# Optimization experiments

Hardware: AMD Instinct MI355X
Metric: run time of the kernel (lower is better)

The kernel has to match this reference:

```python
import jax, jax.numpy as jnp
import numpy as np
from jax import lax

B, C, H, W = 8, 128, 128, 128


def setup_inputs() -> dict:
    key = jax.random.key(0)
    ks = jax.random.split(key, 10)
    s = 0.02
    return {
        "x": jax.random.normal(ks[0], (B, C, H, W), jnp.float32),
        "ln_w": jnp.ones((C,), jnp.float32),
        "ln_b": jnp.zeros((C,), jnp.float32),
        "qkv_w": jax.random.normal(ks[1], (3 * C, C, 1, 1), jnp.float32) * s,
        "qkv_b": jnp.zeros((3 * C,), jnp.float32),
        "dw_w": jax.random.normal(ks[2], (3 * C, 1, 3, 3), jnp.float32) * s,
        "dw_b": jnp.zeros((3 * C,), jnp.float32),
        "proj_w": jax.random.normal(ks[3], (C, C, 1, 1), jnp.float32) * s,
        "proj_b": jnp.zeros((C,), jnp.float32),
        "temp1": jnp.ones((1, 1), jnp.float32),
        "temp2": jnp.ones((1, 1), jnp.float32),
    }


def reference(x, ln_w, ln_b, qkv_w, qkv_b, dw_w, dw_b, proj_w, proj_b, temp1, temp2):
    Cd = x.shape[1]

    def ln(t):  # WithBias LayerNorm over channel dim (unbiased=False var)
        mu = t.mean(axis=1, keepdims=True)
        var = ((t - mu) ** 2).mean(axis=1, keepdims=True)
        return (t - mu) / jnp.sqrt(var + 1e-5) * ln_w[None, :, None, None] + ln_b[None, :, None, None]

    def conv1(t, w, b):  # 1x1 conv
        return jnp.einsum('bchw,oc->bohw', t, w[:, :, 0, 0]) + b[None, :, None, None]

    def dwc(t):  # depthwise 3x3, pad 1
        y = lax.conv_general_dilated(t, dw_w, (1, 1), ((1, 1), (1, 1)),
                                     dimension_numbers=('NCHW', 'OIHW', 'NCHW'),
                                     feature_group_count=t.shape[1])
        return y + dw_b[None, :, None, None]

    def l2n(t):  # F.normalize over last axis, eps=1e-12
        return t / jnp.maximum(jnp.linalg.norm(t, axis=-1, keepdims=True), 1e-12)

    # ---- stage 1: pool over H, attention over W (channel-pooled) ----
    qkv = dwc(conv1(ln(x), qkv_w, qkv_b))
    q1, k1, v1 = qkv[:, :Cd], qkv[:, Cd:2 * Cd], qkv[:, 2 * Cd:]
    q1 = l2n(q1.mean(axis=2)[:, None])           # [B,1,C,W]
    k1 = l2n(k1.max(axis=2)[:, None])            # [B,1,C,W]
    attn1 = jax.nn.softmax(jnp.einsum('bocw,bocv->bowv', q1, k1) * temp1, axis=-1)  # [B,1,W,W]
    out1 = jnp.einsum('bchw,bowv->bchv', v1, attn1)
    out1 = x + conv1(out1, proj_w, proj_b)

    # ---- stage 2: pool over C, attention over H ----
    qkv = dwc(conv1(ln(out1), qkv_w, qkv_b))
    q2, k2, v2 = qkv[:, :Cd], qkv[:, Cd:2 * Cd], qkv[:, 2 * Cd:]
    q2 = l2n(q2.mean(axis=1)[:, None])           # [B,1,H,W]
    k2 = l2n(k2.mean(axis=1)[:, None])           # [B,1,H,W]
    attn2 = jax.nn.softmax(jnp.einsum('bohw,bogw->bohg', q2, k2) * temp2, axis=-1)  # [B,1,H,H]
    out2 = jnp.einsum('bchw,bohg->bcgw', v2, attn2)  # = (v^T @ attn)^T
    out = conv1(out2, proj_w, proj_b) + out1
    return out
```

## Files before the change

kernel.cpp:

```cpp
#include <hip/hip_runtime.h>

typedef __attribute__((ext_vector_type(8))) short bf16x8;
typedef __attribute__((ext_vector_type(4))) float f32x4;
typedef __attribute__((ext_vector_type(4))) unsigned short us4;
typedef __attribute__((ext_vector_type(4))) unsigned int u32x4;

static constexpr int CC = 128, NN = 16384;
static constexpr int O3 = 384;
static constexpr long long CN  = (long long)CC * NN;
static constexpr long long O3N = (long long)O3 * NN;

__device__ __forceinline__ float wave_sum(float v) {
  for (int o = 32; o; o >>= 1) v += __shfl_xor(v, o);
  return v;
}
__device__ __forceinline__ float wave_max(float v) {
  for (int o = 32; o; o >>= 1) v = fmaxf(v, __shfl_xor(v, o));
  return v;
}
__device__ __forceinline__ unsigned short f2bf(float f) {
  unsigned u = __float_as_uint(f);
  u += 0x7FFF + ((u >> 16) & 1);
  return (unsigned short)(u >> 16);
}
__device__ __forceinline__ float bf2f(unsigned short h) {
  return __uint_as_float((unsigned)h << 16);
}

__global__ __launch_bounds__(64) void k_prep(const float* __restrict__ qkvw,
                                             const float* __restrict__ qkvb,
                                             const float* __restrict__ lnw,
                                             const float* __restrict__ lnb,
                                             const float* __restrict__ projw,
                                             unsigned short* __restrict__ Aq,
                                             unsigned short* __restrict__ Ap,
                                             float* __restrict__ Svec,
                                             float* __restrict__ bias2) {
  int o = blockIdx.x, t = threadIdx.x;
  if (o < O3) {
    float w0 = qkvw[o * 128 + t], w1 = qkvw[o * 128 + t + 64];
    unsigned short h0 = f2bf(w0 * lnw[t]), h1 = f2bf(w1 * lnw[t + 64]);
    Aq[o * 128 + t] = h0; Aq[o * 128 + t + 64] = h1;
    float s = wave_sum(bf2f(h0) + bf2f(h1));
    float bs = wave_sum(w0 * lnb[t] + w1 * lnb[t + 64]);
    if (t == 0) { Svec[o] = s; bias2[o] = qkvb[o] + bs; }
  } else {
    int r = o - O3;
    Ap[r * 128 + t] = f2bf(projw[r * 128 + t]);
    Ap[r * 128 + t + 64] = f2bf(projw[r * 128 + t + 64]);
  }
}

__global__ __launch_bounds__(256, 2) void k_qkv_mfma(
    const float* __restrict__ x, const float* __restrict__ mu, const float* __restrict__ rs,
    const unsigned short* __restrict__ Aq, const float* __restrict__ Svec,
    const float* __restrict__ bias2, unsigned short* __restrict__ out, int b0, int useg) {
  __shared__ unsigned short Bs[64 * 128];
  __shared__ float muL[64], rsL[64];
  int bz = blockIdx.z, bg = b0 + bz;
  int n0 = blockIdx.x * 64;
  int t = threadIdx.x, w = t >> 6, l = t & 63;
  int lr = l & 15, lg = l >> 4;
  const float* xb = x + (size_t)bg * CN + n0;

  bf16x8 afr[6][4];
  {
    const unsigned short* Abase = Aq + (size_t)(96 * w + lr) * 128 + lg * 8;
#pragma unroll
    for (int i = 0; i < 6; ++i)
#pragma unroll
      for (int ks = 0; ks < 4; ++ks)
        afr[i][ks] = *(const bf16x8*)&Abase[(size_t)(16 * i) * 128 + ks * 32];
  }

  {
    int n = t & 63, cb = t >> 6;
    float xr[32];
#pragma unroll
    for (int g = 0; g < 4; ++g)
#pragma unroll
      for (int q = 0; q < 8; ++q)
        xr[g * 8 + q] = xb[(size_t)((cb * 4 + g) * 8 + q) * NN + n];
#pragma unroll
    for (int g = 0; g < 4; ++g) {
      int c8 = (cb * 4 + g) * 8;
      unsigned pk[4];
#pragma unroll
      for (int q = 0; q < 4; ++q) {
        unsigned short a = f2bf(xr[g * 8 + 2 * q]);
        unsigned short b = f2bf(xr[g * 8 + 2 * q + 1]);
        pk[q] = (unsigned)a | ((unsigned)b << 16);
      }
      int c8s = c8 ^ ((n & 7) << 3);
      *(u32x4*)&Bs[n * 128 + c8s] = *(const u32x4*)pk;
    }
  }
  __syncthreads();

  if (!useg) {
    int p = t >> 2, sub = t & 3;
    float s1 = 0.f, s2 = 0.f;
#pragma unroll
    for (int b2 = 0; b2 < 4; ++b2) {
      int c8 = (sub * 4 + b2) * 8;
      int c8s = c8 ^ ((p & 7) << 3);
      bf16x8 v = *(const bf16x8*)&Bs[p * 128 + c8s];
#pragma unroll
      for (int q = 0; q < 8; ++q) {
        float f = bf2f((unsigned short)v[q]);
        s1 += f; s2 += f * f;
      }
    }
    s1 += __shfl_xor(s1, 1); s2 += __shfl_xor(s2, 1);
    s1 += __shfl_xor(s1, 2); s2 += __shfl_xor(s2, 2);
    if (sub == 0) {
      float m = s1 * (1.f / 128.f);
      muL[p] = m;
      rsL[p] = rsqrtf(s2 * (1.f / 128.f) - m * m + 1e-5f);
    }
  }
  __syncthreads();

  f32x4 acc[6][4];
#pragma unroll
  for (int i = 0; i < 6; ++i)
#pragma unroll
    for (int j = 0; j < 4; ++j) acc[i][j] = (f32x4){0.f, 0.f, 0.f, 0.f};
#pragma unroll
  for (int ks = 0; ks < 4; ++ks) {
    bf16x8 bfr[4];
#pragma unroll
    for (int j = 0; j < 4; ++j) {
      int row = 16 * j + lr;
      int col = (ks * 32 + lg * 8) ^ ((lr & 7) << 3);
      bfr[j] = *(const bf16x8*)&Bs[row * 128 + col];
    }
#pragma unroll
    for (int i = 0; i < 6; ++i)
#pragma unroll
      for (int j = 0; j < 4; ++j)
        acc[i][j] = __builtin_amdgcn_mfma_f32_16x16x32_bf16(afr[i][ks], bfr[j], acc[i][j], 0, 0, 0);
  }

  float rsv[4], muv[4];
#pragma unroll
  for (int j = 0; j < 4; ++j) {
    int nl = 16 * j + lr;
    if (useg) {
      rsv[j] = rs[(size_t)bg * NN + n0 + nl];
      muv[j] = mu[(size_t)bg * NN + n0 + nl];
    } else {
      rsv[j] = rsL[nl];
      muv[j] = muL[nl];
    }
  }
#pragma unroll
  for (int i = 0; i < 6; ++i) {
    int ob = 96 * w + 16 * i + lg * 4;
    float sv[4], bv[4];
#pragma unroll
    for (int r2 = 0; r2 < 4; ++r2) { sv[r2] = Svec[ob + r2]; bv[r2] = bias2[ob + r2]; }
#pragma unroll
    for (int j = 0; j < 4; ++j) {
      int n = n0 + 16 * j + lr;
      unsigned short* op = out + (size_t)bz * O3N + n;
#pragma unroll
      for (int r2 = 0; r2 < 4; ++r2)
        op[(size_t)(ob + r2) * NN] = f2bf(rsv[j] * (acc[i][j][r2] - muv[j] * sv[r2]) + bv[r2]);
    }
  }
}

__global__ __launch_bounds__(1024) void k_dwc(unsigned short* __restrict__ buf,
                                              const float* __restrict__ dww,
                                              const float* __restrict__ dwb,
                                              float* __restrict__ qm,
                                              float* __restrict__ km,
                                              int b0, int stage) {
  __shared__ unsigned short pl[130 * 144];
  __shared__ float red[32 * 128];
  int o = blockIdx.x, bz = blockIdx.y, bg = b0 + bz;
  int t = threadIdx.x;
  unsigned short* base = buf + (size_t)bz * O3N + (size_t)o * NN;
  unsigned* pl32 = (unsigned*)pl;

  for (int i = t; i < 1168; i += 1024) {
    int idx;
    if (i < 72) idx = i;
    else if (i < 144) idx = 129 * 72 + (i - 72);
    else { int j = i - 144; int row = (j >> 3) + 1; int s = j & 7;
           idx = row * 72 + (s < 4 ? s : 64 + s); }
    pl32[idx] = 0u;
  }
  __syncthreads();
#pragma unroll
  for (int r = 0; r < 2; ++r) {
    int idx = r * 1024 + t;
    int row = idx >> 4, c8 = (idx & 15) * 8;
    *(u32x4*)&pl[(row + 1) * 144 + 8 + c8] = *(const u32x4*)&base[row * 128 + c8];
  }
  __syncthreads();

  const float* wg = dww + o * 9;
  float w00 = wg[0], w01 = wg[1], w02 = wg[2];
  float w10 = wg[3], w11 = wg[4], w12 = wg[5];
  float w20 = wg[6], w21 = wg[7], w22 = wg[8];
  float bias = dwb[o];
  int mode = (stage == 0) ? (o < 128 ? 1 : (o < 256 ? 2 : 0)) : 0;
  int hh0 = t >> 5, w0 = (t & 31) * 4;
  float csum[4] = {0.f, 0.f, 0.f, 0.f};
  float cmax[4] = {-1e30f, -1e30f, -1e30f, -1e30f};

#pragma unroll
  for (int g = 0; g < 4; ++g) {
    int h = g * 32 + hh0;
    float a0 = bias, a1 = bias, a2 = bias, a3 = bias;
#pragma unroll
    for (int dr = 0; dr < 3; ++dr) {
      const unsigned short* rp = &pl[(h + dr) * 144];
      us4 cA = *(const us4*)&rp[w0 + 4];
      us4 cB = *(const us4*)&rp[w0 + 8];
      us4 cC = *(const us4*)&rp[w0 + 12];
      float f0 = bf2f(cA[3]), f1 = bf2f(cB[0]), f2 = bf2f(cB[1]);
      float f3 = bf2f(cB[2]), f4 = bf2f(cB[3]), f5 = bf2f(cC[0]);
      float wr0 = (dr == 0) ? w00 : (dr == 1 ? w10 : w20);
      float wr1 = (dr == 0) ? w01 : (dr == 1 ? w11 : w21);
      float wr2 = (dr == 0) ? w02 : (dr == 1 ? w12 : w22);
      a0 += f0 * wr0 + f1 * wr1 + f2 * wr2;
      a1 += f1 * wr0 + f2 * wr1 + f3 * wr2;
      a2 += f2 * wr0 + f3 * wr1 + f4 * wr2;
      a3 += f3 * wr0 + f4 * wr1 + f5 * wr2;
    }
    if (mode == 0) {
      us4 ov;
      ov[0] = f2bf(a0); ov[1] = f2bf(a1); ov[2] = f2bf(a2); ov[3] = f2bf(a3);
      *(us4*)&base[g * 4096 + t * 4] = ov;
    } else if (mode == 1) {
      csum[0] += a0; csum[1] += a1; csum[2] += a2; csum[3] += a3;
    } else {
      cmax[0] = fmaxf(cmax[0], a0); cmax[1] = fmaxf(cmax[1], a1);
      cmax[2] = fmaxf(cmax[2], a2); cmax[3] = fmaxf(cmax[3], a3);
    }
  }

  if (mode) {
    int j = t >> 5;
#pragma unroll
    for (int dx = 0; dx < 4; ++dx)
      red[j * 128 + w0 + dx] = (mode == 1) ? csum[dx] : cmax[dx];
    __syncthreads();
    if (t < 128) {
      float v = red[t];
      if (mode == 1) {
        for (int jj = 1; jj < 32; ++jj) v += red[jj * 128 + t];
        qm[(size_t)bg * NN + o * 128 + t] = v * (1.f / 128.f);
      } else {
        for (int jj = 1; jj < 32; ++jj) v = fmaxf(v, red[jj * 128 + t]);
        km[(size_t)bg * NN + (o - 128) * 128 + t] = v;
      }
    }
  }
}

__global__ __launch_bounds__(256) void k_reduce2(const unsigned short* __restrict__ qkv,
                                                 float* __restrict__ qm, float* __restrict__ km,
                                                 int b0) {
  int bz = blockIdx.y;
  int n = blockIdx.x * 256 + threadIdx.x;
  const unsigned short* base = qkv + (size_t)bz * O3N + n;
  float sq = 0.f, sk = 0.f;
#pragma unroll 4
  for (int c = 0; c < 128; ++c) {
    sq += bf2f(base[(size_t)c * NN]);
    sk += bf2f(base[(size_t)(c + 128) * NN]);
  }
  size_t off = (size_t)(b0 + bz) * NN + n;
  qm[off] = sq * (1.f / 128.f);
  km[off] = sk * (1.f / 128.f);
}

__global__ void k_norm2(float* __restrict__ qm, float* __restrict__ km, int row0) {
  float* buf = blockIdx.y ? km : qm;
  int r = row0 + blockIdx.x, t = threadIdx.x;
  float* p = buf + (size_t)r * 128;
  float v0 = p[t], v1 = p[t + 64];
  float s = wave_sum(v0 * v0 + v1 * v1);
  float sc = 1.f / fmaxf(sqrtf(s), 1e-12f);
  p[t] = v0 * sc;
  p[t + 64] = v1 * sc;
}

__global__ void k_attn1(const float* __restrict__ qm, const float* __restrict__ km,
                        const float* __restrict__ temp, unsigned short* __restrict__ attnT,
                        int b0) {
  int bg = b0 + blockIdx.y;
  int i = blockIdx.x, t = threadIdx.x;
  const float* qb = qm + (size_t)bg * NN;
  const float* kb = km + (size_t)bg * NN;
  __shared__ float qcol[128];
  __shared__ float wred[2];
  qcol[t] = qb[t * 128 + i];
  __syncthreads();
  float s = 0.f;
#pragma unroll 4
  for (int k = 0; k < 128; ++k) s += qcol[k] * kb[k * 128 + t];
  s *= temp[0];
  int wid = t >> 6, lane = t & 63;
  float mx = wave_max(s);
  if (lane == 0) wred[wid] = mx;
  __syncthreads();
  mx = fmaxf(wred[0], wred[1]);
  float pv = __expf(s - mx);
  __syncthreads();
  float sm = wave_sum(pv);
  if (lane == 0) wred[wid] = sm;
  __syncthreads();
  float denom = wred[0] + wred[1];
  attnT[(size_t)bg * NN + (size_t)t * 128 + i] = f2bf(pv / denom);
}

__global__ void k_attn2(const float* __restrict__ qm, const float* __restrict__ km,
                        const float* __restrict__ temp, unsigned short* __restrict__ attnT,
                        int b0) {
  int bg = b0 + blockIdx.y;
  int i = blockIdx.x, t = threadIdx.x;
  const float* qb = qm + (size_t)bg * NN + i * 128;
  const float* kb = km + (size_t)bg * NN + (size_t)t * 128;
  __shared__ float qrow[128];
  __shared__ float wred[2];
  qrow[t] = qb[t];
  __syncthreads();
  float s = 0.f;
#pragma unroll 4
  for (int w = 0; w < 128; ++w) s += qrow[w] * kb[w];
  s *= temp[0];
  int wid = t >> 6, lane = t & 63;
  float mx = wave_max(s);
  if (lane == 0) wred[wid] = mx;
  __syncthreads();
  mx = fmaxf(wred[0], wred[1]);
  float pv = __expf(s - mx);
  __syncthreads();
  float sm = wave_sum(pv);
  if (lane == 0) wred[wid] = sm;
  __syncthreads();
  float denom = wred[0] + wred[1];
  attnT[(size_t)bg * NN + (size_t)t * 128 + i] = f2bf(pv / denom);
}

__global__ __launch_bounds__(256) void k_apply1_mfma(unsigned short* __restrict__ buf,
                                                     const unsigned short* __restrict__ attnT,
                                                     int b0) {
  __shared__ unsigned short Al[128 * 136];
  __shared__ unsigned short Bl[128 * 136];
  int bz = blockIdx.z, bg = b0 + bz;
  int m0 = blockIdx.x * 128;
  int t = threadIdx.x, w = t >> 6, l = t & 63, lr = l & 15, lg = l >> 4;
  const unsigned short* asrc = buf + (size_t)bz * O3N + (size_t)256 * NN + (size_t)m0 * 128;
  const unsigned short* bsrc = attnT + (size_t)bg * NN;
#pragma unroll
  for (int r = 0; r < 8; ++r) {
    int idx = r * 256 + t;
    int row = idx >> 4, c8 = (idx & 15) * 8;
    *(u32x4*)&Al[row * 136 + c8] = *(const u32x4*)&asrc[row * 128 + c8];
    *(u32x4*)&Bl[row * 136 + c8] = *(const u32x4*)&bsrc[row * 128 + c8];
  }
  __syncthreads();
  f32x4 acc[2][8];
#pragma unroll
  for (int i = 0; i < 2; ++i)
#pragma unroll
    for (int j = 0; j < 8; ++j) acc[i][j] = (f32x4){0.f, 0.f, 0.f, 0.f};
#pragma unroll
  for (int ks = 0; ks < 4; ++ks) {
    bf16x8 bfr[8];
#pragma unroll
    for (int j = 0; j < 8; ++j)
      bfr[j] = *(const bf16x8*)&Bl[(16 * j + lr) * 136 + ks * 32 + lg * 8];
#pragma unroll
    for (int i = 0; i < 2; ++i) {
      bf16x8 afr = *(const bf16x8*)&Al[(32 * w + 16 * i + lr) * 136 + ks * 32 + lg * 8];
#pragma unroll
      for (int j = 0; j < 8; ++j)
        acc[i][j] = __builtin_amdgcn_mfma_f32_16x16x32_bf16(afr, bfr[j], acc[i][j], 0, 0, 0);
    }
  }
  unsigned short* ob = buf + (size_t)bz * O3N;
#pragma unroll
  for (int i = 0; i < 2; ++i)
#pragma unroll
    for (int j = 0; j < 8; ++j)
#pragma unroll
      for (int r2 = 0; r2 < 4; ++r2) {
        int m = m0 + 32 * w + 16 * i + lg * 4 + r2;
        int n = 16 * j + lr;
        ob[(size_t)m * 128 + n] = f2bf(acc[i][j][r2]);
      }
}

__global__ __launch_bounds__(256) void k_apply2_mfma(unsigned short* __restrict__ buf,
                                                     const unsigned short* __restrict__ attnT,
                                                     int b0) {
  __shared__ unsigned short At[128 * 136];
  __shared__ unsigned short Bt[128 * 136];
  int bz = blockIdx.z, bg = b0 + bz, c = blockIdx.x;
  int t = threadIdx.x, w = t >> 6, l = t & 63, lr = l & 15, lg = l >> 4;
  const unsigned short* vsrc = buf + (size_t)bz * O3N + (size_t)(256 + c) * NN;
  const unsigned short* asrc = attnT + (size_t)bg * NN;
#pragma unroll
  for (int r = 0; r < 8; ++r) {
    int idx = r * 256 + t;
    int row = idx >> 4, c8 = (idx & 15) * 8;
    *(u32x4*)&At[row * 136 + c8] = *(const u32x4*)&asrc[row * 128 + c8];
    us4 lo = *(const us4*)&vsrc[row * 128 + c8];
    us4 hi = *(const us4*)&vsrc[row * 128 + c8 + 4];
#pragma unroll
    for (int q = 0; q < 4; ++q) {
      Bt[(c8 + q) * 136 + row] = lo[q];
      Bt[(c8 + 4 + q) * 136 + row] = hi[q];
    }
  }
  __syncthreads();
  f32x4 acc[2][8];
#pragma unroll
  for (int i = 0; i < 2; ++i)
#pragma unroll
    for (int j = 0; j < 8; ++j) acc[i][j] = (f32x4){0.f, 0.f, 0.f, 0.f};
#pragma unroll
  for (int ks = 0; ks < 4; ++ks) {
    bf16x8 bfr[8];
#pragma unroll
    for (int j = 0; j < 8; ++j)
      bfr[j] = *(const bf16x8*)&Bt[(16 * j + lr) * 136 + ks * 32 + lg * 8];
#pragma unroll
    for (int i = 0; i < 2; ++i) {
      bf16x8 afr = *(const bf16x8*)&At[(32 * w + 16 * i + lr) * 136 + ks * 32 + lg * 8];
#pragma unroll
      for (int j = 0; j < 8; ++j)
        acc[i][j] = __builtin_amdgcn_mfma_f32_16x16x32_bf16(afr, bfr[j], acc[i][j], 0, 0, 0);
    }
  }
  unsigned short* ob = buf + (size_t)bz * O3N + (size_t)c * NN;
#pragma unroll
  for (int i = 0; i < 2; ++i)
#pragma unroll
    for (int j = 0; j < 8; ++j)
#pragma unroll
      for (int r2 = 0; r2 < 4; ++r2) {
        int g = 32 * w + 16 * i + lg * 4 + r2;
        int n = 16 * j + lr;
        ob[(size_t)g * 128 + n] = f2bf(acc[i][j][r2]);
      }
}

__global__ __launch_bounds__(256) void k_proj_mfma(
    const unsigned short* __restrict__ tin, const unsigned short* __restrict__ Ap,
    const float* __restrict__ pb, const float* __restrict__ res,
    float* __restrict__ dst, float* __restrict__ mu, float* __restrict__ rs,
    int b0, int do_stats) {
  __shared__ unsigned short Bs2[64 * 128];
  __shared__ float red1[64 * 17];
  __shared__ float red2[64 * 17];
  int bz = blockIdx.z, bg = b0 + bz;
  int n0 = blockIdx.x * 64;
  int t = threadIdx.x, w = t >> 6, l = t & 63, lr = l & 15, lg = l >> 4;
  const unsigned short* tb = tin + (size_t)bz * O3N + n0;

  bf16x8 afr[2][4];
  {
    const unsigned short* Abase = Ap + (size_t)(32 * w + lr) * 128 + lg * 8;
#pragma unroll
    for (int i = 0; i < 2; ++i)
#pragma unroll
      for (int ks = 0; ks < 4; ++ks)
        afr[i][ks] = *(const bf16x8*)&Abase[(size_t)(16 * i) * 128 + ks * 32];
  }

  {
    int n = t & 63, cb = t >> 6;
    unsigned short vr[32];
#pragma unroll
    for (int g = 0; g < 4; ++g)
#pragma unroll
      for (int q = 0; q < 8; ++q)
        vr[g * 8 + q] = tb[(size_t)((cb * 4 + g) * 8 + q) * NN + n];
#pragma unroll
    for (int g = 0; g < 4; ++g) {
      int c8 = (cb * 4 + g) * 8;
      unsigned pk[4];
#pragma unroll
      for (int q = 0; q < 4; ++q)
        pk[q] = (unsigned)vr[g * 8 + 2 * q] | ((unsigned)vr[g * 8 + 2 * q + 1] << 16);
      int c8s = c8 ^ ((n & 7) << 3);
      *(u32x4*)&Bs2[n * 128 + c8s] = *(const u32x4*)pk;
    }
  }
  __syncthreads();

  f32x4 acc[2][4];
#pragma unroll
  for (int i = 0; i < 2; ++i)
#pragma unroll
    for (int j = 0; j < 4; ++j) acc[i][j] = (f32x4){0.f, 0.f, 0.f, 0.f};

#pragma unroll
  for (int ks = 0; ks < 4; ++ks) {
    bf16x8 bfr[4];
#pragma unroll
    for (int j = 0; j < 4; ++j) {
      int row = 16 * j + lr;
      int col = (ks * 32 + lg * 8) ^ ((lr & 7) << 3);
      bfr[j] = *(const bf16x8*)&Bs2[row * 128 + col];
    }
#pragma unroll
    for (int i = 0; i < 2; ++i)
#pragma unroll
      for (int j = 0; j < 4; ++j)
        acc[i][j] = __builtin_amdgcn_mfma_f32_16x16x32_bf16(afr[i][ks], bfr[j], acc[i][j], 0, 0, 0);
  }

  float s1p[4] = {0.f, 0.f, 0.f, 0.f}, s2p[4] = {0.f, 0.f, 0.f, 0.f};
#pragma unroll
  for (int i = 0; i < 2; ++i) {
    int ob = 32 * w + 16 * i + lg * 4;
    float bv[4];
#pragma unroll
    for (int r2 = 0; r2 < 4; ++r2) bv[r2] = pb[ob + r2];
#pragma unroll
    for (int j = 0; j < 4; ++j) {
      int n = n0 + 16 * j + lr;
#pragma unroll
      for (int r2 = 0; r2 < 4; ++r2) {
        size_t off = (size_t)bg * CN + (size_t)(ob + r2) * NN + n;
        float val = acc[i][j][r2] + bv[r2] + res[off];
        dst[off] = val;
        s1p[j] += val;
        s2p[j] += val * val;
      }
    }
  }
  if (do_stats) {
#pragma unroll
    for (int j = 0; j < 4; ++j) {
      red1[(16 * j + lr) * 17 + (w * 4 + lg)] = s1p[j];
      red2[(16 * j + lr) * 17 + (w * 4 + lg)] = s2p[j];
    }
    __syncthreads();
    if (t < 64) {
      float s1 = 0.f, s2 = 0.f;
#pragma unroll
      for (int kk = 0; kk < 16; ++kk) { s1 += red1[t * 17 + kk]; s2 += red2[t * 17 + kk]; }
      float m = s1 * (1.f / 128.f);
      float var = s2 * (1.f / 128.f) - m * m;
      mu[(size_t)bg * NN + n0 + t] = m;
      rs[(size_t)bg * NN + n0 + t] = rsqrtf(var + 1e-5f);
    }
  }
}

extern "C" void kernel_launch(void* const* d_in, const int* in_sizes, int n_in,
                              void* d_out, int out_size, void* d_ws, size_t ws_size,
                              hipStream_t stream) {
  (void)in_sizes; (void)n_in; (void)out_size;
  const float* x     = (const float*)d_in[0];
  const float* lnw   = (const float*)d_in[1];
  const float* lnb   = (const float*)d_in[2];
  const float* qkvw  = (const float*)d_in[3];
  const float* qkvb  = (const float*)d_in[4];
  const float* dww   = (const float*)d_in[5];
  const float* dwb   = (const float*)d_in[6];
  const float* projw = (const float*)d_in[7];
  const float* projb = (const float*)d_in[8];
  const float* temp1 = (const float*)d_in[9];
  const float* temp2 = (const float*)d_in[10];
  float* out = (float*)d_out;
  float* ws = (float*)d_ws;

  auto needBytes = [&](int nb) {
    return ((size_t)nb * (O3N / 2) + 4ull * 131072 + 65536 + 768 + 24576 + 8192) * 4;
  };
  int NB = 8;
  while (NB > 1 && ws_size < needBytes(NB)) NB >>= 1;
  if (ws_size < needBytes(1)) return;

  unsigned short* convbuf = (unsigned short*)ws;
  float* mu = ws + (size_t)NB * (O3N / 2);
  float* rs = mu + 131072;
  float* qm = rs + 131072;
  float* km = qm + 131072;
  unsigned short* attnT = (unsigned short*)(km + 131072);
  float* Svec  = (float*)(attnT + 8ull * NN);
  float* bias2 = Svec + 384;
  unsigned short* Aq = (unsigned short*)(bias2 + 384);
  unsigned short* Ap = Aq + 49152;

  k_prep<<<512, 64, 0, stream>>>(qkvw, qkvb, lnw, lnb, projw, Aq, Ap, Svec, bias2);

  for (int stage = 0; stage < 2; ++stage) {
    const float* src = stage ? out : x;
    for (int b0 = 0; b0 < 8; b0 += NB) {
      k_qkv_mfma<<<dim3(256, 1, NB), 256, 0, stream>>>(src, mu, rs, Aq, Svec, bias2, convbuf,
                                                       b0, stage);
      k_dwc<<<dim3(384, NB), 1024, 0, stream>>>(convbuf, dww, dwb, qm, km, b0, stage);
      if (stage == 1)
        k_reduce2<<<dim3(64, NB), 256, 0, stream>>>(convbuf, qm, km, b0);
      k_norm2<<<dim3(NB * 128, 2), 64, 0, stream>>>(qm, km, b0 * 128);
      if (stage == 0)
        k_attn1<<<dim3(128, NB), 128, 0, stream>>>(qm, km, temp1, attnT, b0);
      else
        k_attn2<<<dim3(128, NB), 128, 0, stream>>>(qm, km, temp2, attnT, b0);
      if (stage == 0)
        k_apply1_mfma<<<dim3(128, 1, NB), 256, 0, stream>>>(convbuf, attnT, b0);
      else
        k_apply2_mfma<<<dim3(128, 1, NB), 256, 0, stream>>>(convbuf, attnT, b0);
      const float* resp = stage ? out : x;
      k_proj_mfma<<<dim3(256, 1, NB), 256, 0, stream>>>(convbuf, Ap, projb, resp, out,
                                                        mu, rs, b0, stage == 0 ? 1 : 0);
    }
  }
}
```

Measured before the change: 311.7 us.

## Stage weight tiles in LDS and split QKV GEMM across output halves

The QKV 1x1-conv kernel no longer holds all 384x128 weight fragments in registers. Each block now covers 192 output channels, staged into padded shared memory, and the grid doubles along that axis. The proj kernel likewise loads its weight matrix into padded LDS instead of registers. The aim is to cut register pressure and raise occupancy, at the cost of reading and LayerNorm-converting each x tile twice and adding LDS traffic for A fragments.

```diff
diff --git a/kernel.cpp b/kernel.cpp
--- a/kernel.cpp
+++ b/kernel.cpp
@@ -51,28 +51,29 @@
   }
 }
 
-__global__ __launch_bounds__(256, 2) void k_qkv_mfma(
+__global__ __launch_bounds__(256) void k_qkv_mfma(
     const float* __restrict__ x, const float* __restrict__ mu, const float* __restrict__ rs,
     const unsigned short* __restrict__ Aq, const float* __restrict__ Svec,
     const float* __restrict__ bias2, unsigned short* __restrict__ out, int b0, int useg) {
+  __shared__ unsigned short As[192 * 136];
   __shared__ unsigned short Bs[64 * 128];
   __shared__ float muL[64], rsL[64];
   int bz = blockIdx.z, bg = b0 + bz;
-  int n0 = blockIdx.x * 64;
+  int m0 = blockIdx.x * 192;
+  int n0 = blockIdx.y * 64;
   int t = threadIdx.x, w = t >> 6, l = t & 63;
   int lr = l & 15, lg = l >> 4;
   const float* xb = x + (size_t)bg * CN + n0;
 
-  bf16x8 afr[6][4];
   {
-    const unsigned short* Abase = Aq + (size_t)(96 * w + lr) * 128 + lg * 8;
-#pragma unroll
-    for (int i = 0; i < 6; ++i)
-#pragma unroll
-      for (int ks = 0; ks < 4; ++ks)
-        afr[i][ks] = *(const bf16x8*)&Abase[(size_t)(16 * i) * 128 + ks * 32];
-  }
-
+    const unsigned short* Asrc = Aq + (size_t)m0 * 128;
+#pragma unroll
+    for (int r = 0; r < 12; ++r) {
+      int v = r * 256 + t;
+      int m = v >> 4, c8 = (v & 15) * 8;
+      *(u32x4*)&As[m * 136 + c8] = *(const u32x4*)&Asrc[m * 128 + c8];
+    }
+  }
   {
     int n = t & 63, cb = t >> 6;
     float xr[32];
@@ -121,9 +122,9 @@
   }
   __syncthreads();
 
-  f32x4 acc[6][4];
-#pragma unroll
-  for (int i = 0; i < 6; ++i)
+  f32x4 acc[3][4];
+#pragma unroll
+  for (int i = 0; i < 3; ++i)
 #pragma unroll
     for (int j = 0; j < 4; ++j) acc[i][j] = (f32x4){0.f, 0.f, 0.f, 0.f};
 #pragma unroll
@@ -136,10 +137,12 @@
       bfr[j] = *(const bf16x8*)&Bs[row * 128 + col];
     }
 #pragma unroll
-    for (int i = 0; i < 6; ++i)
+    for (int i = 0; i < 3; ++i) {
+      bf16x8 afr = *(const bf16x8*)&As[(48 * w + 16 * i + lr) * 136 + ks * 32 + lg * 8];
 #pragma unroll
       for (int j = 0; j < 4; ++j)
-        acc[i][j] = __builtin_amdgcn_mfma_f32_16x16x32_bf16(afr[i][ks], bfr[j], acc[i][j], 0, 0, 0);
+        acc[i][j] = __builtin_amdgcn_mfma_f32_16x16x32_bf16(afr, bfr[j], acc[i][j], 0, 0, 0);
+    }
   }
 
   float rsv[4], muv[4];
@@ -155,8 +158,8 @@
     }
   }
 #pragma unroll
-  for (int i = 0; i < 6; ++i) {
-    int ob = 96 * w + 16 * i + lg * 4;
+  for (int i = 0; i < 3; ++i) {
+    int ob = m0 + 48 * w + 16 * i + lg * 4;
     float sv[4], bv[4];
 #pragma unroll
     for (int r2 = 0; r2 < 4; ++r2) { sv[r2] = Svec[ob + r2]; bv[r2] = bias2[ob + r2]; }
@@ -458,6 +461,7 @@
     const float* __restrict__ pb, const float* __restrict__ res,
     float* __restrict__ dst, float* __restrict__ mu, float* __restrict__ rs,
     int b0, int do_stats) {
+  __shared__ unsigned short Al[128 * 136];
   __shared__ unsigned short Bs2[64 * 128];
   __shared__ float red1[64 * 17];
   __shared__ float red2[64 * 17];
@@ -466,16 +470,12 @@
   int t = threadIdx.x, w = t >> 6, l = t & 63, lr = l & 15, lg = l >> 4;
   const unsigned short* tb = tin + (size_t)bz * O3N + n0;
 
-  bf16x8 afr[2][4];
-  {
-    const unsigned short* Abase = Ap + (size_t)(32 * w + lr) * 128 + lg * 8;
-#pragma unroll
-    for (int i = 0; i < 2; ++i)
-#pragma unroll
-      for (int ks = 0; ks < 4; ++ks)
-        afr[i][ks] = *(const bf16x8*)&Abase[(size_t)(16 * i) * 128 + ks * 32];
-  }
-
+#pragma unroll
+  for (int r = 0; r < 8; ++r) {
+    int v = r * 256 + t;
+    int m = v >> 4, c8 = (v & 15) * 8;
+    *(u32x4*)&Al[m * 136 + c8] = *(const u32x4*)&Ap[m * 128 + c8];
+  }
   {
     int n = t & 63, cb = t >> 6;
     unsigned short vr[32];
@@ -513,10 +513,12 @@
       bfr[j] = *(const bf16x8*)&Bs2[row * 128 + col];
     }
 #pragma unroll
-    for (int i = 0; i < 2; ++i)
+    for (int i = 0; i < 2; ++i) {
+      bf16x8 afr = *(const bf16x8*)&Al[(32 * w + 16 * i + lr) * 136 + ks * 32 + lg * 8];
 #pragma unroll
       for (int j = 0; j < 4; ++j)
-        acc[i][j] = __builtin_amdgcn_mfma_f32_16x16x32_bf16(afr[i][ks], bfr[j], acc[i][j], 0, 0, 0);
+        acc[i][j] = __builtin_amdgcn_mfma_f32_16x16x32_bf16(afr, bfr[j], acc[i][j], 0, 0, 0);
+    }
   }
 
   float s1p[4] = {0.f, 0.f, 0.f, 0.f}, s2p[4] = {0.f, 0.f, 0.f, 0.f};
@@ -599,7 +601,7 @@
   for (int stage = 0; stage < 2; ++stage) {
     const float* src = stage ? out : x;
     for (int b0 = 0; b0 < 8; b0 += NB) {
-      k_qkv_mfma<<<dim3(256, 1, NB), 256, 0, stream>>>(src, mu, rs, Aq, Svec, bias2, convbuf,
+      k_qkv_mfma<<<dim3(2, 256, NB), 256, 0, stream>>>(src, mu, rs, Aq, Svec, bias2, convbuf,
                                                        b0, stage);
       k_dwc<<<dim3(384, NB), 1024, 0, stream>>>(convbuf, dww, dwb, qm, km, b0, stage);
       if (stage == 1)
```

Result: no change. 310.6 us (-0.4%).
